# Optimization experiments

Hardware: AMD Instinct MI355X
Metric: run time of the kernel (lower is better)

Reference implementation:

```python
import jax, jax.numpy as jnp
import numpy as np

B, S, T = 256, 1024, 64

def setup_inputs() -> dict:
    key = jax.random.key(0)
    k1, k2, k3, k4, k5 = jax.random.split(key, 5)
    emissions = jax.random.normal(k1, (B, S, T), dtype=jnp.float32)
    tags = jax.random.randint(k2, (B, S), 0, T, dtype=jnp.int64)
    mask = jnp.ones((B, S), dtype=jnp.int32)
    transitions = jax.random.normal(k3, (T, T), dtype=jnp.float32) * 0.1
    start_transitions = jax.random.normal(k4, (T,), dtype=jnp.float32) * 0.1
    end_transitions = jax.random.normal(k5, (T,), dtype=jnp.float32) * 0.1
    return {"emissions": emissions, "tags": tags, "mask": mask,
            "transitions": transitions, "start_transitions": start_transitions,
            "end_transitions": end_transitions}


def _gold_score(emissions, tags, maskf, transitions, start_transitions, end_transitions):
    # emission score at each gold tag: [B, S]
    emit = jnp.take_along_axis(emissions, tags[:, :, None], axis=2)[:, :, 0]
    # transition score between consecutive gold tags: [B, S-1]
    trans = transitions[tags[:, :-1], tags[:, 1:]]
    score = start_transitions[tags[:, 0]] + emit[:, 0]
    score = score + jnp.sum((trans + emit[:, 1:]) * maskf[:, 1:], axis=1)
    last_pos = maskf.astype(jnp.int32).sum(axis=1) - 1           # [B]
    last_tags = jnp.take_along_axis(tags, last_pos[:, None], axis=1)[:, 0]
    return score + end_transitions[last_tags]


def _log_partition(emissions, maskf, transitions, start_transitions, end_transitions):
    alpha0 = start_transitions[None, :] + emissions[:, 0]        # [B, T]

    def step(alpha, xs):
        emit_t, m_t = xs                                         # [B, T], [B]
        # scores[b, i, j] = alpha[b, i] + transitions[i, j] + emit_t[b, j]
        scores = alpha[:, :, None] + transitions[None, :, :] + emit_t[:, None, :]
        new_alpha = jax.nn.logsumexp(scores, axis=1)             # [B, T]
        alpha = jnp.where(m_t[:, None] > 0, new_alpha, alpha)
        return alpha, None

    xs = (jnp.swapaxes(emissions[:, 1:], 0, 1), jnp.swapaxes(maskf[:, 1:], 0, 1))
    alpha, _ = jax.lax.scan(step, alpha0, xs)
    return jax.nn.logsumexp(alpha + end_transitions[None, :], axis=1)  # [B]


def reference(emissions, tags, mask, transitions, start_transitions, end_transitions):
    maskf = mask.astype(emissions.dtype)
    log_Z = _log_partition(emissions, maskf, transitions, start_transitions, end_transitions)
    score = _gold_score(emissions, tags, maskf, transitions, start_transitions, end_transitions)
    return jnp.mean(log_Z - score)
```

## Files before the change

kernel.cpp:

```cpp
#include <hip/hip_runtime.h>

#define Bn 256
#define Sn 1024
#define Tn 64
#define NCH 16
#define BURN 64
#define SLAB 4
#define RAWSTR 260
#define CROW 72
#define MROW 129
#define LN2 0.69314718055994531f
#define L7LN2 4.8520302639196169f

typedef __attribute__((ext_vector_type(8))) short short8;
typedef __attribute__((ext_vector_type(4))) float f32x4;

__device__ __forceinline__ unsigned short f2bf_rne(float f) {
  unsigned u = __float_as_uint(f);
  u = (u + 0x7fffu + ((u >> 16) & 1u)) >> 16;
  return (unsigned short)u;
}
__device__ __forceinline__ unsigned pk2(float hi, float lo) {
  return __builtin_amdgcn_perm(__float_as_uint(hi), __float_as_uint(lo), 0x07060302);
}
__device__ __forceinline__ unsigned pke(float a, float b) {
  return (unsigned)f2bf_rne(__expf(a - L7LN2)) |
         ((unsigned)f2bf_rne(__expf(b - L7LN2)) << 16);
}
__device__ __forceinline__ void gl_lds16(const void* src, void* dst) {
  __builtin_amdgcn_global_load_lds(
      (const __attribute__((address_space(1))) void*)src,
      (__attribute__((address_space(3))) void*)dst, 16, 0, 0);
}
__device__ __forceinline__ void gl_lds4(const void* src, void* dst) {
  __builtin_amdgcn_global_load_lds(
      (const __attribute__((address_space(1))) void*)src,
      (__attribute__((address_space(3))) void*)dst, 4, 0, 0);
}

__global__ __launch_bounds__(128, 1) void crf_scan(
    const float* __restrict__ em, const int* __restrict__ tags,
    const int* __restrict__ mask, const float* __restrict__ trans,
    const float* __restrict__ startt, const float* __restrict__ endt,
    float* __restrict__ wsL, float* __restrict__ wsGold,
    int* __restrict__ wsM, float* __restrict__ wsSE, float* __restrict__ wsA,
    int* __restrict__ cnt, float* __restrict__ out) {
  const int g = blockIdx.x & 15;
  const int c = blockIdx.x >> 4;
  const int Wc = (c == 0) ? 0 : BURN;
  const int Lc = (c == NCH - 1) ? 63 : 64;
  const int TOT = Wc + Lc;
  const int NSLAB = (TOT + SLAB - 1) / SLAB;
  const int t0 = 64 * c + 1;
  const int tstart = t0 - Wc;
  const int tid = threadIdx.x;
  const int wid = tid >> 6;
  const int lane = tid & 63;
  const int m = lane & 15;
  const int q = lane >> 4;

  __shared__ __align__(16) float rawS[2][16 * RAWSTR];
  __shared__ __align__(16) short convS[2][SLAB * 16 * CROW];
  __shared__ __align__(16) short alpha[16 * CROW];
  __shared__ int maskL[16 * MROW];
  __shared__ int lastF;
  __shared__ float eend[64];
  __shared__ float rsum[2];

  short8 a00, a01, a10, a11, a20, a21, a30, a31;
  uint2 st0, st1, st2, st3;
  float Slog = 0.f;
  int K = 0, NL = 0;
  const f32x4 zero4 = {0.f, 0.f, 0.f, 0.f};

  auto issue_slab = [&](int s) {
    if (s >= NSLAB) return;
    float* dstb = rawS[s & 1];
    const int rem = TOT - 4 * s;
    if (rem >= SLAB) {
      for (int mm = 0; mm < 16; ++mm)
        gl_lds16(em + ((size_t)(16 * g + mm) * Sn + tstart + 4 * s) * 64 + lane * 4,
                 dstb + mm * RAWSTR);
    } else {
      for (int mm = 0; mm < 16; ++mm)
        for (int u = 0; u < rem; ++u)
          gl_lds4(em + ((size_t)(16 * g + mm) * Sn + tstart + 4 * s + u) * 64 + lane,
                  dstb + mm * RAWSTR + u * 64);
    }
  };
  auto convert_slab = [&](int s) {
    if (s >= NSLAB) return;
    const int mm = lane & 15, seg = lane >> 4;
    const float* rp = rawS[s & 1] + mm * RAWSTR + seg * 16;
    short* cb = convS[s & 1];
    const int vu = min(SLAB, TOT - 4 * s);
    for (int u = 0; u < vu; ++u) {
      float4 v0 = *(const float4*)(rp + u * 64 + 0);
      float4 v1 = *(const float4*)(rp + u * 64 + 4);
      float4 v2 = *(const float4*)(rp + u * 64 + 8);
      float4 v3 = *(const float4*)(rp + u * 64 + 12);
      uint4 w0, w1;
      w0.x = pke(v0.x, v0.y); w0.y = pke(v0.z, v0.w);
      w0.z = pke(v1.x, v1.y); w0.w = pke(v1.z, v1.w);
      w1.x = pke(v2.x, v2.y); w1.y = pke(v2.z, v2.w);
      w1.z = pke(v3.x, v3.y); w1.w = pke(v3.z, v3.w);
      short* cw = cb + (u * 16 + mm) * CROW + seg * 16;
      *(uint4*)(cw) = w0;
      *(uint4*)(cw + 8) = w1;
    }
  };

  if (wid == 0) {
#define LOADA(tm, kc, dst) { \
    _Pragma("unroll") for (int jj = 0; jj < 8; ++jj) { \
      int kk = kc * 32 + q * 8 + jj; \
      dst[jj] = (short)f2bf_rne(__expf(trans[kk * Tn + 16 * tm + m])); \
    } }
    LOADA(0, 0, a00) LOADA(0, 1, a01) LOADA(1, 0, a10) LOADA(1, 1, a11)
    LOADA(2, 0, a20) LOADA(2, 1, a21) LOADA(3, 0, a30) LOADA(3, 1, a31)
#undef LOADA
    if (c == 0) {
#define INIT0(tm, ss) { \
      float4 sv = *(const float4*)(startt + 16 * tm + 4 * q); \
      float4 ev = *(const float4*)(em + (size_t)(16 * g + m) * Sn * Tn + 16 * tm + 4 * q); \
      ss.x = (unsigned)f2bf_rne(__expf(sv.x + ev.x)) | \
             ((unsigned)f2bf_rne(__expf(sv.y + ev.y)) << 16); \
      ss.y = (unsigned)f2bf_rne(__expf(sv.z + ev.z)) | \
             ((unsigned)f2bf_rne(__expf(sv.w + ev.w)) << 16); }
      INIT0(0, st0) INIT0(1, st1) INIT0(2, st2) INIT0(3, st3)
#undef INIT0
    } else {
      st0.x = 0x3F803F80u; st0.y = 0x3F803F80u; st1 = st0; st2 = st0; st3 = st0;
    }
    issue_slab(0);
  } else {
    for (int mm = 0; mm < 16; ++mm) {
      gl_lds4(mask + (size_t)(16 * g + mm) * Sn + tstart + lane,
              (void*)(maskL + mm * MROW));
      bool special = (c == NCH - 1) && (g == 15) && (mm == 15);
      if (!special)
        gl_lds4(mask + (size_t)(16 * g + mm) * Sn + tstart + 64 + lane,
                (void*)(maskL + mm * MROW + 64));
    }
    {
      const int bm = 16 * g + m;
      const int qq = q;
      const int* tg = tags + (size_t)bm * Sn;
      const int* mkb = mask + (size_t)bm * Sn;
      const float* emb = em + (size_t)bm * Sn * Tn;
      float acc = 0.f;
      int cntg = 0;
      #pragma unroll 4
      for (int i = 0; i < 16; ++i) {
        int t = t0 + qq + 4 * i;
        bool ok = t < t0 + Lc;
        int ts = ok ? t : t0;
        int mv = mkb[ts];
        int tp = tg[ts - 1], tc = tg[ts];
        float w = trans[tp * Tn + tc] + emb[(size_t)ts * Tn + tc];
        acc += (ok && mv) ? w : 0.f;
        cntg += ok ? mv : 0;
      }
      acc += __shfl_xor(acc, 16); acc += __shfl_xor(acc, 32);
      cntg += __shfl_xor(cntg, 16); cntg += __shfl_xor(cntg, 32);
      if (qq == 0) { wsGold[c * 256 + bm] = acc; wsM[c * 256 + bm] = cntg; }
    }
    if (c == NCH - 1 && g == 15) {
      int t = tstart + 64 + lane;
      if (t < Sn) maskL[15 * MROW + 64 + lane] = mask[(size_t)255 * Sn + t];
    }
  }
  asm volatile("s_waitcnt vmcnt(0)" ::: "memory");
  __syncthreads();

  if (wid == 0) issue_slab(1);
  else convert_slab(0);
  asm volatile("s_waitcnt vmcnt(0)" ::: "memory");
  __syncthreads();

#define UNP(ss, x0, x1, x2, x3) \
  x0 = __uint_as_float(ss.x << 16); x1 = __uint_as_float(ss.x & 0xffff0000u); \
  x2 = __uint_as_float(ss.y << 16); x3 = __uint_as_float(ss.y & 0xffff0000u);

  for (int r = 0; r < NSLAB; ++r) {
    if (wid == 0) {
      issue_slab(r + 2);
      const short* cbase = convS[r & 1];
      short* arow = alpha + m * CROW;
      #pragma unroll
      for (int u = 0; u < SLAB; ++u) {
        const int tt = 4 * r + u;
        if (tt < TOT) {
          if (((r & 1) == 0) && u == 0) {
            float x00, x01, x02, x03, x10, x11, x12, x13;
            float x20, x21, x22, x23, x30, x31, x32, x33;
            UNP(st0, x00, x01, x02, x03) UNP(st1, x10, x11, x12, x13)
            UNP(st2, x20, x21, x22, x23) UNP(st3, x30, x31, x32, x33)
            float sm = (((x00 + x01) + (x02 + x03)) + ((x10 + x11) + (x12 + x13)))
                     + (((x20 + x21) + (x22 + x23)) + ((x30 + x31) + (x32 + x33)));
            sm += __shfl_xor(sm, 16); sm += __shfl_xor(sm, 32);
            if (c != 0 && tt == BURN) { Slog = __logf(sm); K = 0; NL = 0; }
            int k = 127 - (int)((__float_as_uint(sm) >> 23) & 255u);
            float fk = __uint_as_float((unsigned)(127 + k) << 23);
            x00 *= fk; x01 *= fk; x02 *= fk; x03 *= fk;
            x10 *= fk; x11 *= fk; x12 *= fk; x13 *= fk;
            x20 *= fk; x21 *= fk; x22 *= fk; x23 *= fk;
            x30 *= fk; x31 *= fk; x32 *= fk; x33 *= fk;
            st0.x = pk2(x01, x00); st0.y = pk2(x03, x02);
            st1.x = pk2(x11, x10); st1.y = pk2(x13, x12);
            st2.x = pk2(x21, x20); st2.y = pk2(x23, x22);
            st3.x = pk2(x31, x30); st3.y = pk2(x33, x32);
            K += k;
          }
          const short* ep = cbase + (u * 16 + m) * CROW;
          uint2 eu0 = *(const uint2*)(ep + 0 + 4 * q);
          uint2 eu1 = *(const uint2*)(ep + 16 + 4 * q);
          uint2 eu2 = *(const uint2*)(ep + 32 + 4 * q);
          uint2 eu3 = *(const uint2*)(ep + 48 + 4 * q);
          int mv = maskL[m * MROW + tt];
          *(uint2*)(arow + 4 * q) = st0;
          *(uint2*)(arow + 16 + 4 * q) = st1;
          *(uint2*)(arow + 32 + 4 * q) = st2;
          *(uint2*)(arow + 48 + 4 * q) = st3;
          short8 b0 = *(const short8*)(arow + q * 8);
          short8 b1 = *(const short8*)(arow + 32 + q * 8);
          f32x4 d0 = __builtin_amdgcn_mfma_f32_16x16x32_bf16(a00, b0, zero4, 0, 0, 0);
          f32x4 d1 = __builtin_amdgcn_mfma_f32_16x16x32_bf16(a10, b0, zero4, 0, 0, 0);
          f32x4 d2 = __builtin_amdgcn_mfma_f32_16x16x32_bf16(a20, b0, zero4, 0, 0, 0);
          f32x4 d3 = __builtin_amdgcn_mfma_f32_16x16x32_bf16(a30, b0, zero4, 0, 0, 0);
          d0 = __builtin_amdgcn_mfma_f32_16x16x32_bf16(a01, b1, d0, 0, 0, 0);
          d1 = __builtin_amdgcn_mfma_f32_16x16x32_bf16(a11, b1, d1, 0, 0, 0);
          d2 = __builtin_amdgcn_mfma_f32_16x16x32_bf16(a21, b1, d2, 0, 0, 0);
          d3 = __builtin_amdgcn_mfma_f32_16x16x32_bf16(a31, b1, d3, 0, 0, 0);
          const bool live = (mv != 0);
#define EPI(dd, eu, ss) { \
          float e0 = __uint_as_float(eu.x << 16); \
          float e1 = __uint_as_float(eu.x & 0xffff0000u); \
          float e2 = __uint_as_float(eu.y << 16); \
          float e3 = __uint_as_float(eu.y & 0xffff0000u); \
          unsigned nx = pk2(dd[1] * e1, dd[0] * e0); \
          unsigned ny = pk2(dd[3] * e3, dd[2] * e2); \
          ss.x = live ? nx : ss.x; \
          ss.y = live ? ny : ss.y; }
          EPI(d0, eu0, st0) EPI(d1, eu1, st1) EPI(d2, eu2, st2) EPI(d3, eu3, st3)
#undef EPI
          NL += (live && tt >= Wc) ? 1 : 0;
        }
      }
    } else {
      convert_slab(r + 1);
    }
    asm volatile("s_waitcnt vmcnt(0)" ::: "memory");
    __syncthreads();
  }

  if (wid == 0) {
    float x00, x01, x02, x03, x10, x11, x12, x13;
    float x20, x21, x22, x23, x30, x31, x32, x33;
    UNP(st0, x00, x01, x02, x03) UNP(st1, x10, x11, x12, x13)
    UNP(st2, x20, x21, x22, x23) UNP(st3, x30, x31, x32, x33)
    float sm = (((x00 + x01) + (x02 + x03)) + ((x10 + x11) + (x12 + x13)))
             + (((x20 + x21) + (x22 + x23)) + ((x30 + x31) + (x32 + x33)));
    sm += __shfl_xor(sm, 16); sm += __shfl_xor(sm, 32);
    const int bm = 16 * g + m;
    float L = __logf(sm) - Slog + LN2 * (float)(7 * NL - K);
    if (q == 0) wsL[c * 256 + bm] = L;
    if (c == NCH - 1) {
      if (q == 0) wsSE[bm] = __logf(sm);
      wsA[(0 + 4 * q + 0) * 256 + bm] = x00;  wsA[(0 + 4 * q + 1) * 256 + bm] = x01;
      wsA[(0 + 4 * q + 2) * 256 + bm] = x02;  wsA[(0 + 4 * q + 3) * 256 + bm] = x03;
      wsA[(16 + 4 * q + 0) * 256 + bm] = x10; wsA[(16 + 4 * q + 1) * 256 + bm] = x11;
      wsA[(16 + 4 * q + 2) * 256 + bm] = x12; wsA[(16 + 4 * q + 3) * 256 + bm] = x13;
      wsA[(32 + 4 * q + 0) * 256 + bm] = x20; wsA[(32 + 4 * q + 1) * 256 + bm] = x21;
      wsA[(32 + 4 * q + 2) * 256 + bm] = x22; wsA[(32 + 4 * q + 3) * 256 + bm] = x23;
      wsA[(48 + 4 * q + 0) * 256 + bm] = x30; wsA[(48 + 4 * q + 1) * 256 + bm] = x31;
      wsA[(48 + 4 * q + 2) * 256 + bm] = x32; wsA[(48 + 4 * q + 3) * 256 + bm] = x33;
    }
  }
#undef UNP

  __threadfence();
  __syncthreads();
  if (tid == 0) lastF = (atomicAdd(cnt, 1) == 255) ? 1 : 0;
  __syncthreads();
  if (lastF) {
    __threadfence();
    if (tid < 64) eend[tid] = __expf(endt[tid]);
    __syncthreads();
    float vsum = 0.f;
    for (int bb = tid; bb < Bn; bb += 128) {
      float sumL = 0.f, gold = 0.f;
      int msum = 0;
      #pragma unroll
      for (int cc = 0; cc < NCH; ++cc) {
        sumL += wsL[cc * 256 + bb];
        gold += wsGold[cc * 256 + bb];
        msum += wsM[cc * 256 + bb];
      }
      msum += mask[(size_t)bb * Sn];
      float se = 0.f;
      for (int jj = 0; jj < Tn; ++jj) se += wsA[jj * 256 + bb] * eend[jj];
      float logZ = sumL + __logf(se) - wsSE[bb];
      int tg0 = tags[(size_t)bb * Sn];
      int lastTag = tags[(size_t)bb * Sn + (msum - 1)];
      gold += startt[tg0] + em[(size_t)bb * Sn * Tn + tg0] + endt[lastTag];
      vsum += logZ - gold;
    }
    #pragma unroll
    for (int o = 32; o > 0; o >>= 1) vsum += __shfl_xor(vsum, o, 64);
    if (lane == 0) rsum[wid] = vsum;
    __syncthreads();
    if (tid == 0) out[0] = (rsum[0] + rsum[1]) * (1.0f / Bn);
  }
}

extern "C" void kernel_launch(void* const* d_in, const int* in_sizes, int n_in,
                              void* d_out, int out_size, void* d_ws, size_t ws_size,
                              hipStream_t stream) {
  const float* em     = (const float*)d_in[0];
  const int*   tags   = (const int*)d_in[1];
  const int*   mask   = (const int*)d_in[2];
  const float* trans  = (const float*)d_in[3];
  const float* startt = (const float*)d_in[4];
  const float* endt   = (const float*)d_in[5];
  float* out = (float*)d_out;

  float* wsL    = (float*)d_ws;
  float* wsGold = wsL + NCH * 256;
  int*   wsM    = (int*)(wsGold + NCH * 256);
  float* wsSE   = (float*)(wsM + NCH * 256);
  float* wsA    = wsSE + 256;
  int*   cnt    = (int*)(wsA + 64 * 256);

  hipMemsetAsync(cnt, 0, sizeof(int), stream);
  crf_scan<<<256, 128, 0, stream>>>(em, tags, mask, trans, startt, endt,
                                    wsL, wsGold, wsM, wsSE, wsA, cnt, out);
}
```

Measured before the change: 174.4 us.

## Permute tag ordering so MFMA output feeds next step's B operand directly

Reorders the tag index mapping across the transition matrix A operand, emission conversion layout, initial state and final workspace writes so that each lane's MFMA accumulator outputs line up with the B-operand fragment it needs next step. This removes the per-timestep LDS round-trip through the alpha buffer (four stores plus two vector loads) on the serial recurrence critical path. The cost is more complex index permutations, which must stay consistent everywhere the state layout is touched.

```diff
diff --git a/kernel.cpp b/kernel.cpp
--- a/kernel.cpp
+++ b/kernel.cpp
@@ -26,6 +26,11 @@
 __device__ __forceinline__ unsigned pke(float a, float b) {
   return (unsigned)f2bf_rne(__expf(a - L7LN2)) |
          ((unsigned)f2bf_rne(__expf(b - L7LN2)) << 16);
+}
+__device__ __forceinline__ short8 cat4(uint2 a, uint2 b) {
+  union { unsigned u[4]; short8 s; } x;
+  x.u[0] = a.x; x.u[1] = a.y; x.u[2] = b.x; x.u[3] = b.y;
+  return x.s;
 }
 __device__ __forceinline__ void gl_lds16(const void* src, void* dst) {
   __builtin_amdgcn_global_load_lds(
@@ -58,10 +63,10 @@
   const int lane = tid & 63;
   const int m = lane & 15;
   const int q = lane >> 4;
+  const int mrow = 8 * (m >> 2) + (m & 3);
 
   __shared__ __align__(16) float rawS[2][16 * RAWSTR];
   __shared__ __align__(16) short convS[2][SLAB * 16 * CROW];
-  __shared__ __align__(16) short alpha[16 * CROW];
   __shared__ int maskL[16 * MROW];
   __shared__ int lastF;
   __shared__ float eend[64];
@@ -94,19 +99,20 @@
     const float* rp = rawS[s & 1] + mm * RAWSTR + seg * 16;
     short* cb = convS[s & 1];
     const int vu = min(SLAB, TOT - 4 * s);
+    const int base = (seg >> 1) * 32 + (seg & 1) * 8;
     for (int u = 0; u < vu; ++u) {
       float4 v0 = *(const float4*)(rp + u * 64 + 0);
       float4 v1 = *(const float4*)(rp + u * 64 + 4);
       float4 v2 = *(const float4*)(rp + u * 64 + 8);
       float4 v3 = *(const float4*)(rp + u * 64 + 12);
-      uint4 w0, w1;
-      w0.x = pke(v0.x, v0.y); w0.y = pke(v0.z, v0.w);
-      w0.z = pke(v1.x, v1.y); w0.w = pke(v1.z, v1.w);
-      w1.x = pke(v2.x, v2.y); w1.y = pke(v2.z, v2.w);
-      w1.z = pke(v3.x, v3.y); w1.w = pke(v3.z, v3.w);
-      short* cw = cb + (u * 16 + mm) * CROW + seg * 16;
-      *(uint4*)(cw) = w0;
-      *(uint4*)(cw + 8) = w1;
+      uint4 o0, o1;
+      o0.x = pke(v0.x, v0.y); o0.y = pke(v0.z, v0.w);
+      o1.x = pke(v1.x, v1.y); o1.y = pke(v1.z, v1.w);
+      o0.z = pke(v2.x, v2.y); o0.w = pke(v2.z, v2.w);
+      o1.z = pke(v3.x, v3.y); o1.w = pke(v3.z, v3.w);
+      short* cw = cb + (u * 16 + mm) * CROW + base;
+      *(uint4*)(cw) = o0;
+      *(uint4*)(cw + 16) = o1;
     }
   };
 
@@ -114,20 +120,21 @@
 #define LOADA(tm, kc, dst) { \
     _Pragma("unroll") for (int jj = 0; jj < 8; ++jj) { \
       int kk = kc * 32 + q * 8 + jj; \
-      dst[jj] = (short)f2bf_rne(__expf(trans[kk * Tn + 16 * tm + m])); \
+      dst[jj] = (short)f2bf_rne(__expf(trans[kk * Tn + (32 * ((tm) >> 1) + 4 * ((tm) & 1) + mrow)])); \
     } }
     LOADA(0, 0, a00) LOADA(0, 1, a01) LOADA(1, 0, a10) LOADA(1, 1, a11)
     LOADA(2, 0, a20) LOADA(2, 1, a21) LOADA(3, 0, a30) LOADA(3, 1, a31)
 #undef LOADA
     if (c == 0) {
-#define INIT0(tm, ss) { \
-      float4 sv = *(const float4*)(startt + 16 * tm + 4 * q); \
-      float4 ev = *(const float4*)(em + (size_t)(16 * g + m) * Sn * Tn + 16 * tm + 4 * q); \
+#define INIT0(off, ss) { \
+      float4 sv = *(const float4*)(startt + (off)); \
+      float4 ev = *(const float4*)(em + (size_t)(16 * g + m) * Sn * Tn + (off)); \
       ss.x = (unsigned)f2bf_rne(__expf(sv.x + ev.x)) | \
              ((unsigned)f2bf_rne(__expf(sv.y + ev.y)) << 16); \
       ss.y = (unsigned)f2bf_rne(__expf(sv.z + ev.z)) | \
              ((unsigned)f2bf_rne(__expf(sv.w + ev.w)) << 16); }
-      INIT0(0, st0) INIT0(1, st1) INIT0(2, st2) INIT0(3, st3)
+      INIT0(8 * q, st0) INIT0(8 * q + 4, st1)
+      INIT0(32 + 8 * q, st2) INIT0(36 + 8 * q, st3)
 #undef INIT0
     } else {
       st0.x = 0x3F803F80u; st0.y = 0x3F803F80u; st1 = st0; st2 = st0; st3 = st0;
@@ -186,7 +193,6 @@
     if (wid == 0) {
       issue_slab(r + 2);
       const short* cbase = convS[r & 1];
-      short* arow = alpha + m * CROW;
       #pragma unroll
       for (int u = 0; u < SLAB; ++u) {
         const int tt = 4 * r + u;
@@ -218,12 +224,8 @@
           uint2 eu2 = *(const uint2*)(ep + 32 + 4 * q);
           uint2 eu3 = *(const uint2*)(ep + 48 + 4 * q);
           int mv = maskL[m * MROW + tt];
-          *(uint2*)(arow + 4 * q) = st0;
-          *(uint2*)(arow + 16 + 4 * q) = st1;
-          *(uint2*)(arow + 32 + 4 * q) = st2;
-          *(uint2*)(arow + 48 + 4 * q) = st3;
-          short8 b0 = *(const short8*)(arow + q * 8);
-          short8 b1 = *(const short8*)(arow + 32 + q * 8);
+          short8 b0 = cat4(st0, st1);
+          short8 b1 = cat4(st2, st3);
           f32x4 d0 = __builtin_amdgcn_mfma_f32_16x16x32_bf16(a00, b0, zero4, 0, 0, 0);
           f32x4 d1 = __builtin_amdgcn_mfma_f32_16x16x32_bf16(a10, b0, zero4, 0, 0, 0);
           f32x4 d2 = __builtin_amdgcn_mfma_f32_16x16x32_bf16(a20, b0, zero4, 0, 0, 0);
@@ -267,14 +269,14 @@
     if (q == 0) wsL[c * 256 + bm] = L;
     if (c == NCH - 1) {
       if (q == 0) wsSE[bm] = __logf(sm);
-      wsA[(0 + 4 * q + 0) * 256 + bm] = x00;  wsA[(0 + 4 * q + 1) * 256 + bm] = x01;
-      wsA[(0 + 4 * q + 2) * 256 + bm] = x02;  wsA[(0 + 4 * q + 3) * 256 + bm] = x03;
-      wsA[(16 + 4 * q + 0) * 256 + bm] = x10; wsA[(16 + 4 * q + 1) * 256 + bm] = x11;
-      wsA[(16 + 4 * q + 2) * 256 + bm] = x12; wsA[(16 + 4 * q + 3) * 256 + bm] = x13;
-      wsA[(32 + 4 * q + 0) * 256 + bm] = x20; wsA[(32 + 4 * q + 1) * 256 + bm] = x21;
-      wsA[(32 + 4 * q + 2) * 256 + bm] = x22; wsA[(32 + 4 * q + 3) * 256 + bm] = x23;
-      wsA[(48 + 4 * q + 0) * 256 + bm] = x30; wsA[(48 + 4 * q + 1) * 256 + bm] = x31;
-      wsA[(48 + 4 * q + 2) * 256 + bm] = x32; wsA[(48 + 4 * q + 3) * 256 + bm] = x33;
+      wsA[(8 * q + 0) * 256 + bm] = x00;  wsA[(8 * q + 1) * 256 + bm] = x01;
+      wsA[(8 * q + 2) * 256 + bm] = x02;  wsA[(8 * q + 3) * 256 + bm] = x03;
+      wsA[(8 * q + 4) * 256 + bm] = x10;  wsA[(8 * q + 5) * 256 + bm] = x11;
+      wsA[(8 * q + 6) * 256 + bm] = x12;  wsA[(8 * q + 7) * 256 + bm] = x13;
+      wsA[(32 + 8 * q + 0) * 256 + bm] = x20; wsA[(32 + 8 * q + 1) * 256 + bm] = x21;
+      wsA[(32 + 8 * q + 2) * 256 + bm] = x22; wsA[(32 + 8 * q + 3) * 256 + bm] = x23;
+      wsA[(36 + 8 * q + 0) * 256 + bm] = x30; wsA[(36 + 8 * q + 1) * 256 + bm] = x31;
+      wsA[(36 + 8 * q + 2) * 256 + bm] = x32; wsA[(36 + 8 * q + 3) * 256 + bm] = x33;
     }
   }
 #undef UNP
```

Measured after the change: 166.3 us. 1.05x faster.
